# Performance work log

Measured on AMD Instinct MI355X. Metric: run time of the kernel, lower is better.

## Reference

```python
import jax, jax.numpy as jnp
import numpy as np
import math

DIM = 256; SEQ = 2048; BSZ = 32; NI = 128; NS = 4; ITERS = 3

def _ln(x, g, b):
    m = x.mean(-1, keepdims=True)
    v = ((x - m) ** 2).mean(-1, keepdims=True)
    return (x - m) / jnp.sqrt(v + 1e-5) * g + b

def _norm(x):
    # torch F.normalize: x / ||x||.clamp_min(1e-12)
    return x / jnp.clip(jnp.linalg.norm(x, axis=-1, keepdims=True), 1e-12, None)

def setup_inputs() -> dict:
    key = jax.random.key(0)
    ks = jax.random.split(key, 16)
    def w(k, shape, s=0.02):
        return jax.random.normal(k, shape, jnp.float32) * s
    return {
        'tokens': jax.random.normal(ks[0], (BSZ, SEQ, DIM), jnp.float32),
        'cls_embed': jax.random.normal(ks[1], (BSZ, DIM), jnp.float32),
        'intent_queries': jax.random.normal(ks[2], (NI, DIM), jnp.float32),
        'noise': jax.random.normal(ks[3], (NI, BSZ, NS, DIM), jnp.float32),
        'Wk': w(ks[4], (DIM, DIM)), 'bk': jnp.zeros(DIM, jnp.float32),
        'Wv': w(ks[5], (DIM, DIM)), 'bv': jnp.zeros(DIM, jnp.float32),
        'Wqs': w(ks[6], (DIM, DIM)), 'bqs': jnp.zeros(DIM, jnp.float32),
        'Wqi': w(ks[7], (DIM, DIM)), 'bqi': jnp.zeros(DIM, jnp.float32),
        'ln1_g': jnp.ones(DIM, jnp.float32), 'ln1_b': jnp.zeros(DIM, jnp.float32),
        'ln2_g': jnp.ones(DIM, jnp.float32), 'ln2_b': jnp.zeros(DIM, jnp.float32),
        'Wf1': w(ks[8], (DIM, 2 * DIM)), 'bf1': jnp.zeros(2 * DIM, jnp.float32),
        'Wf2': w(ks[9], (2 * DIM, DIM)), 'bf2': jnp.zeros(DIM, jnp.float32),
        'slot_mu': w(ks[10], (1, NS, DIM)),  # randn*0.02
        'slot_sigma': jnp.ones((1, NS, DIM), jnp.float32) * 0.1,
        'alpha': jnp.float32(1.0),
        'temperature': jnp.float32(1.0),
    }

def reference(tokens, cls_embed, intent_queries, noise, Wk, bk, Wv, bv,
              Wqs, bqs, Wqi, bqi, ln1_g, ln1_b, ln2_g, ln2_b,
              Wf1, bf1, Wf2, bf2, slot_mu, slot_sigma, alpha, temperature):
    scale = 1.0 / math.sqrt(DIM)
    # k/v are identical across the per-intent loop in the original -> compute once
    k = tokens @ Wk + bk  # [B,S,D]
    v = tokens @ Wv + bv  # [B,S,D]
    cls_n = _norm(cls_embed)  # [B,D]

    def per_intent(q, eps):  # q: [D], eps: [B,NS,D]
        qn = _norm(q)
        q_intent = (q @ Wqi + bqi)[None, None, :]  # broadcast over [B,NS,:]
        slots = slot_mu[0] + eps * slot_sigma[0]   # [B,NS,D]
        for _ in range(ITERS):
            q_slot = slots @ Wqs + bqs + q_intent
            logit = jnp.einsum('bnd,bsd->bns', q_slot, k) * scale
            attn = jax.nn.softmax(logit, axis=-1)
            upd = jnp.einsum('bns,bsd->bnd', attn, v)
            slots = _ln(slots + upd, ln1_g, ln1_b)
            h = _ln(slots, ln2_g, ln2_b)
            slots = slots + jax.nn.gelu(h @ Wf1 + bf1, approximate=False) @ Wf2 + bf2
        sn = _norm(slots)                               # [B,NS,D]
        a = jax.nn.softmax(jnp.einsum('bnd,d->bn', sn, qn), axis=-1)
        summ = jnp.einsum('bn,bnd->bd', a, slots)       # slot_summary
        fused = cls_n + alpha * _norm(summ)
        return fused @ qn                               # [B]

    scores = jax.vmap(per_intent)(intent_queries, noise)  # [NI,B]
    logits = scores.T / jnp.maximum(temperature, 1e-4)    # [B,NI]
    return logits
```

## Files before the change

### kernel.cpp

```cpp
#include <hip/hip_runtime.h>
#include <math.h>

#define BSZ 32
#define NI  128

typedef __attribute__((ext_vector_type(8))) _Float16 f16x8;
typedef __attribute__((ext_vector_type(4))) _Float16 f16x4;
typedef __attribute__((ext_vector_type(4))) float    f32x4;

#define MFMA16(a, b, c) __builtin_amdgcn_mfma_f32_16x16x32_f16((a), (b), (c), 0, 0, 0)

#define GLL(g, l) __builtin_amdgcn_global_load_lds(                          \
    (const __attribute__((address_space(1))) void*)(g),                      \
    (__attribute__((address_space(3))) void*)(l), 16, 0, 0)

#define LGKM_BAR() do {                                                      \
    asm volatile("s_waitcnt lgkmcnt(0)" ::: "memory");                       \
    __builtin_amdgcn_sched_barrier(0);                                       \
    __builtin_amdgcn_s_barrier();                                            \
    __builtin_amdgcn_sched_barrier(0); } while (0)

__device__ inline float dot4f(float4 a, float4 b) {
    return a.x * b.x + a.y * b.y + a.z * b.z + a.w * b.w;
}

__device__ inline float4* slp(float* base, int r, int c) {
    return (float4*)(base + r * 256 + ((((c) >> 2) ^ (r & 7)) << 2));
}

__device__ inline void tpose64(const float* __restrict__ src, int Csrc,
                               _Float16* __restrict__ dstT, int KT,
                               int r0, int c0, _Float16 (*tbuf)[72], int tid)
{
#pragma unroll
    for (int it = 0; it < 4; it++) {
        int idx = tid + it * 256;
        int rr = idx >> 4, c4 = idx & 15;
        float4 w = *(const float4*)(src + (size_t)(r0 + rr) * Csrc + c0 + c4 * 4);
        tbuf[c4 * 4 + 0][rr] = (_Float16)w.x;
        tbuf[c4 * 4 + 1][rr] = (_Float16)w.y;
        tbuf[c4 * 4 + 2][rr] = (_Float16)w.z;
        tbuf[c4 * 4 + 3][rr] = (_Float16)w.w;
    }
    __syncthreads();
#pragma unroll
    for (int it = 0; it < 2; it++) {
        int idx = tid + it * 256;
        int orr = idx >> 3, oc8 = idx & 7;
        int n = c0 + orr;
        size_t tile = (size_t)(n >> 4) * KT + (r0 >> 5) + (oc8 >> 2);
        *(f16x8*)(dstT + tile * 512 + (n & 15) * 32 + (oc8 & 3) * 8) = *(const f16x8*)&tbuf[orr][oc8 * 8];
    }
}

__global__ __launch_bounds__(256) void prep(
    const float* __restrict__ Wk, const float* __restrict__ Wv,
    const float* __restrict__ Wqs, const float* __restrict__ Wf1,
    const float* __restrict__ Wf2,
    const float* __restrict__ intent_q, const float* __restrict__ Wqi,
    const float* __restrict__ bqi, const float* __restrict__ bqs,
    const float* __restrict__ cls_embed,
    _Float16* __restrict__ wkT, _Float16* __restrict__ wvT,
    _Float16* __restrict__ wqsT, _Float16* __restrict__ wf1T,
    _Float16* __restrict__ wf2T,
    float* __restrict__ qint2, float* __restrict__ qn, float* __restrict__ clsn)
{
    __shared__ _Float16 tbuf[64][72];
    __shared__ float buf[256];
    __shared__ float red[4];
    const int t = threadIdx.x, blk = blockIdx.x;
    const int lane = t & 63, w = t >> 6;

    if (blk < 112) {
        if (blk < 16)       tpose64(Wk, 256, wkT, 8, (blk >> 2) * 64, (blk & 3) * 64, tbuf, t);
        else if (blk < 32)  { int tt = blk - 16; tpose64(Wv, 256, wvT, 8, (tt >> 2) * 64, (tt & 3) * 64, tbuf, t); }
        else if (blk < 48)  { int tt = blk - 32; tpose64(Wqs, 256, wqsT, 8, (tt >> 2) * 64, (tt & 3) * 64, tbuf, t); }
        else if (blk < 80)  { int tt = blk - 48; tpose64(Wf1, 512, wf1T, 8, (tt & 3) * 64, (tt >> 2) * 64, tbuf, t); }
        else                { int tt = blk - 80; tpose64(Wf2, 256, wf2T, 16, (tt >> 2) * 64, (tt & 3) * 64, tbuf, t); }
    } else if (blk < 240) {
        int i = blk - 112;
        float x = intent_q[(size_t)i * 256 + t];
        buf[t] = x;
        float ss = x * x;
#pragma unroll
        for (int m = 1; m < 64; m <<= 1) ss += __shfl_xor(ss, m, 64);
        if (lane == 0) red[w] = ss;
        __syncthreads();
        float tot = red[0] + red[1] + red[2] + red[3];
        qn[(size_t)i * 256 + t] = x / fmaxf(sqrtf(tot), 1e-12f);
        float acc = bqi[t] + bqs[t];
        for (int e = 0; e < 256; e += 4) {
            const float4 q4 = *(const float4*)&buf[e];
            acc += q4.x * Wqi[(size_t)(e + 0) * 256 + t];
            acc += q4.y * Wqi[(size_t)(e + 1) * 256 + t];
            acc += q4.z * Wqi[(size_t)(e + 2) * 256 + t];
            acc += q4.w * Wqi[(size_t)(e + 3) * 256 + t];
        }
        qint2[(size_t)i * 256 + t] = acc;
    } else {
        int b = blk - 240;
        float x = cls_embed[(size_t)b * 256 + t];
        float ss = x * x;
#pragma unroll
        for (int m = 1; m < 64; m <<= 1) ss += __shfl_xor(ss, m, 64);
        if (lane == 0) red[w] = ss;
        __syncthreads();
        float tot = red[0] + red[1] + red[2] + red[3];
        clsn[(size_t)b * 256 + t] = x / fmaxf(sqrtf(tot), 1e-12f);
    }
}

__global__ __launch_bounds__(512, 2) void kvf_k(
    const float* __restrict__ tokens,
    const _Float16* __restrict__ wkT, const _Float16* __restrict__ wvT,
    const float* __restrict__ bk, const float* __restrict__ bv,
    _Float16* __restrict__ kT, _Float16* __restrict__ vT)
{
    __shared__ __align__(16) _Float16 Sb[2][8192];

    const int t = threadIdx.x, lane = t & 63, w = t >> 6;
    const int l15 = lane & 15, quad = lane >> 4;
    const int lofs = l15 * 32 + quad * 8;
    const int lofsA = ((l15 * 4 + quad) ^ ((l15 >> 1) & 7)) * 8;
    const int bx = blockIdx.x;
    const int b = bx & 31, chunk = bx >> 5;

    f16x8 wk[2][8], wv[2][8];
#pragma unroll
    for (int j = 0; j < 2; j++)
#pragma unroll
        for (int ks = 0; ks < 8; ks++) {
            wk[j][ks] = *(const f16x8*)(wkT + ((size_t)(2 * w + j) * 8 + ks) * 512 + lofs);
            wv[j][ks] = *(const f16x8*)(wvT + ((size_t)(2 * w + j) * 8 + ks) * 512 + lofs);
        }
    f32x4 bi0 = *(const f32x4*)(bk + w * 32 + quad * 4);
    f32x4 bi1 = *(const f32x4*)(bk + w * 32 + 16 + quad * 4);
    const float bv0 = bv[(2 * w) * 16 + l15];
    const float bv1 = bv[(2 * w + 1) * 16 + l15];

    const int rr = t >> 5, d8 = t & 31;
    const float* tbase = tokens + ((size_t)b * 2048 + chunk * 256) * 256 + rr * 256 + d8 * 8;
    const int mskW = ((rr >> 1) & 7) ^ (((d8 >> 2) & 3) << 1);
    const int wofs0 = (d8 >> 2) * 512 + (((rr * 4 + (d8 & 3)) ^ mskW) * 8);
    const int wofs1 = wofs0 + 8 * 512;

    float4 pa0, pa1, pb0, pb1;

#define KVF_LOADS(P) do {                                                    \
        const float* sp_ = tbase + (size_t)(P) * 8192;                       \
        pa0 = *(const float4*)(sp_);                                         \
        pa1 = *(const float4*)(sp_ + 4);                                     \
        pb0 = *(const float4*)(sp_ + 4096);                                  \
        pb1 = *(const float4*)(sp_ + 4100);                                  \
    } while (0)

#define KVF_STAGE(BUF) do {                                                  \
        f16x8 h0, h1;                                                        \
        h0[0] = (_Float16)pa0.x; h0[1] = (_Float16)pa0.y;                    \
        h0[2] = (_Float16)pa0.z; h0[3] = (_Float16)pa0.w;                    \
        h0[4] = (_Float16)pa1.x; h0[5] = (_Float16)pa1.y;                    \
        h0[6] = (_Float16)pa1.z; h0[7] = (_Float16)pa1.w;                    \
        h1[0] = (_Float16)pb0.x; h1[1] = (_Float16)pb0.y;                    \
        h1[2] = (_Float16)pb0.z; h1[3] = (_Float16)pb0.w;                    \
        h1[4] = (_Float16)pb1.x; h1[5] = (_Float16)pb1.y;                    \
        h1[6] = (_Float16)pb1.z; h1[7] = (_Float16)pb1.w;                    \
        *(f16x8*)((BUF) + wofs0) = h0;                                       \
        *(f16x8*)((BUF) + wofs1) = h1;                                       \
    } while (0)

    KVF_LOADS(0);
    KVF_STAGE(&Sb[0][0]);
    LGKM_BAR();

    for (int p = 0; p < 8; p++) {
        if (p < 7) KVF_LOADS(p + 1);
        __builtin_amdgcn_sched_barrier(0);

        const _Float16* lb = &Sb[p & 1][0];
        const int stg0 = chunk * 16 + p * 2;
        const int sp = chunk * 8 + p;

        f16x8 a[2][8];
#pragma unroll
        for (int st = 0; st < 2; st++)
#pragma unroll
            for (int ks = 0; ks < 8; ks++)
                a[st][ks] = *(const f16x8*)(lb + (st * 8 + ks) * 512 + (lofsA ^ ((ks & 3) * 16)));

#pragma unroll
        for (int st = 0; st < 2; st++) {
            f32x4 c0 = {0.f, 0.f, 0.f, 0.f}, c1 = {0.f, 0.f, 0.f, 0.f};
#pragma unroll
            for (int ks = 0; ks < 8; ks++) {
                c0 = MFMA16(wk[0][ks], a[st][ks], c0);
                c1 = MFMA16(wk[1][ks], a[st][ks], c1);
            }
            f16x4 p0, p1;
#pragma unroll
            for (int reg = 0; reg < 4; reg++) {
                p0[reg] = (_Float16)(c0[reg] + bi0[reg]);
                p1[reg] = (_Float16)(c1[reg] + bi1[reg]);
            }
            _Float16* tp = kT + ((size_t)(b * 128 + stg0 + st) * 8 + w) * 512 + l15 * 32;
            *(f16x4*)(tp + (quad >> 1) * 8 + (quad & 1) * 4) = p0;
            *(f16x4*)(tp + (2 + (quad >> 1)) * 8 + (quad & 1) * 4) = p1;
        }

#pragma unroll
        for (int j = 0; j < 2; j++) {
            f32x4 c0 = {0.f, 0.f, 0.f, 0.f}, c1 = {0.f, 0.f, 0.f, 0.f};
#pragma unroll
            for (int ks = 0; ks < 8; ks++) {
                c0 = MFMA16(a[0][ks], wv[j][ks], c0);
                c1 = MFMA16(a[1][ks], wv[j][ks], c1);
            }
            const float bb = j ? bv1 : bv0;
            f16x4 p0, p1;
#pragma unroll
            for (int reg = 0; reg < 4; reg++) {
                p0[reg] = (_Float16)(c0[reg] + bb);
                p1[reg] = (_Float16)(c1[reg] + bb);
            }
            _Float16* tp = vT + ((size_t)(b * 16 + 2 * w + j) * 64 + sp) * 512 + l15 * 32;
            *(f16x4*)(tp + (quad >> 1) * 8 + (quad & 1) * 4) = p0;
            *(f16x4*)(tp + (2 + (quad >> 1)) * 8 + (quad & 1) * 4) = p1;
        }

        if (p < 7) {
            KVF_STAGE(&Sb[(p + 1) & 1][0]);
            LGKM_BAR();
        }
    }
#undef KVF_LOADS
#undef KVF_STAGE
}

__global__ __launch_bounds__(256) void slots_init(
    const float* __restrict__ noise, const float* __restrict__ slot_mu,
    const float* __restrict__ slot_sigma, float* __restrict__ slots,
    _Float16* __restrict__ slotsT)
{
    int idx = blockIdx.x * 256 + threadIdx.x;
    int row = idx >> 5, d8 = idx & 31;
    int b = row >> 9, i = (row >> 2) & 127, n = row & 3;
    int d = d8 * 8;
    const float* mp = slot_mu + n * 256 + d;
    const float* sp = slot_sigma + n * 256 + d;
    const float* np = noise + (((size_t)i * BSZ + b) * 4 + n) * 256 + d;
    float4 o0, o1;
    {
        float4 mu = *(const float4*)mp, sg = *(const float4*)sp, ns = *(const float4*)np;
        o0.x = mu.x + ns.x * sg.x; o0.y = mu.y + ns.y * sg.y;
        o0.z = mu.z + ns.z * sg.z; o0.w = mu.w + ns.w * sg.w;
    }
    {
        float4 mu = *(const float4*)(mp + 4), sg = *(const float4*)(sp + 4), ns = *(const float4*)(np + 4);
        o1.x = mu.x + ns.x * sg.x; o1.y = mu.y + ns.y * sg.y;
        o1.z = mu.z + ns.z * sg.z; o1.w = mu.w + ns.w * sg.w;
    }
    *(float4*)(slots + (size_t)row * 256 + d) = o0;
    *(float4*)(slots + (size_t)row * 256 + d + 4) = o1;
    f16x8 h;
    h[0] = (_Float16)o0.x; h[1] = (_Float16)o0.y; h[2] = (_Float16)o0.z; h[3] = (_Float16)o0.w;
    h[4] = (_Float16)o1.x; h[5] = (_Float16)o1.y; h[6] = (_Float16)o1.z; h[7] = (_Float16)o1.w;
    *(f16x8*)(slotsT + ((size_t)(row >> 4) * 8 + (d8 >> 2)) * 512 + (row & 15) * 32 + (d8 & 3) * 8) = h;
}

__global__ __launch_bounds__(256) void qslot_k(
    const _Float16* __restrict__ slotsT, const _Float16* __restrict__ wqsT,
    const float* __restrict__ qint2, _Float16* __restrict__ qsT)
{
    const int tid = threadIdx.x, lane = tid & 63, wv = tid >> 6;
    const int l15 = lane & 15, quad = lane >> 4;
    const int lofs = l15 * 32 + quad * 8;
    const int bx = blockIdx.x, rb = bx >> 2, dq = bx & 3;
    const int rt = rb * 4 + wv;
    const int gr0 = rt * 16;

    f16x8 bs[8];
#pragma unroll
    for (int ks = 0; ks < 8; ks++)
        bs[ks] = *(const f16x8*)(slotsT + ((size_t)rt * 8 + ks) * 512 + lofs);
    const int iq = ((gr0 + l15) & 511) >> 2;
#pragma unroll
    for (int dt = 0; dt < 4; dt++) {
        int dti = dq * 4 + dt;
        f32x4 c = {0.f, 0.f, 0.f, 0.f};
#pragma unroll
        for (int ks = 0; ks < 8; ks++)
            c = MFMA16(*(const f16x8*)(wqsT + ((size_t)dti * 8 + ks) * 512 + lofs), bs[ks], c);
        float4 qi = *(const float4*)(qint2 + (size_t)iq * 256 + dti * 16 + quad * 4);
        f16x4 o;
#pragma unroll
        for (int reg = 0; reg < 4; reg++) o[reg] = (_Float16)((c[reg] + qi[reg]) * 0.0625f);
        *(f16x4*)(qsT + ((size_t)rt * 8 + (dti >> 1)) * 512 + l15 * 32
                  + ((dti & 1) * 2 + (quad >> 1)) * 8 + (quad & 1) * 4) = o;
    }
}

__global__ __launch_bounds__(512, 2) void attn_k(
    const _Float16* __restrict__ qsT, const _Float16* __restrict__ kT,
    const _Float16* __restrict__ vT,
    _Float16* __restrict__ Opart, float* __restrict__ psum4)
{
    __shared__ __align__(16) _Float16 Kb[2][16384];
    __shared__ __align__(16) _Float16 Vb[16384];
    __shared__ __align__(16) _Float16 pb[8][2304];

    const int tid = threadIdx.x, lane = tid & 63, wv = tid >> 6;
    const int l15 = lane & 15, quad = lane >> 4;
    const int lofs = l15 * 32 + quad * 8;
    const int lofsA = ((l15 * 4 + quad) ^ ((l15 >> 1) & 7)) * 8;
    const int lnsw = (lane ^ ((lane >> 3) & 7)) * 8;
    const int bx = blockIdx.x;
    const int b = bx & 31, rb = (bx >> 5) & 1, sk = bx >> 6;
    const int gr0 = b * 512 + rb * 256 + wv * 32;
    const int rt_q = gr0 >> 4;

    _Float16* pw = pb[wv];

    const _Float16* kSrc = kT + ((size_t)(b * 128 + sk * 32) * 8) * 512;

    {
        const _Float16* src = kSrc + (size_t)(wv * 4) * 512 + lnsw;
        _Float16* dst = &Kb[0][(wv * 4) * 512 + lane * 8];
#pragma unroll
        for (int j = 0; j < 4; j++) GLL(src + j * 512, dst + j * 512);
    }

    f16x8 q[2][8];
#pragma unroll
    for (int m = 0; m < 2; m++)
#pragma unroll
        for (int ks = 0; ks < 8; ks++)
            q[m][ks] = *(const f16x8*)(qsT + ((size_t)(rt_q + m) * 8 + ks) * 512 + lofs);

    f32x4 O[2][16];
#pragma unroll
    for (int m = 0; m < 2; m++)
#pragma unroll
        for (int dt = 0; dt < 16; dt++) O[m][dt] = (f32x4){0.f, 0.f, 0.f, 0.f};
    float ps[2][4] = {{0.f, 0.f, 0.f, 0.f}, {0.f, 0.f, 0.f, 0.f}};

    asm volatile("s_waitcnt vmcnt(0)" ::: "memory");
    __builtin_amdgcn_s_barrier();
    __builtin_amdgcn_sched_barrier(0);

    for (int s = 0; s < 8; s++) {
        const int cur = s & 1;

        {
            const int seg0 = wv * 4;
#pragma unroll
            for (int j = 0; j < 4; j++) {
                const int seg = seg0 + j;
                const _Float16* src = vT
                    + ((size_t)(b * 16 + (seg >> 1)) * 64 + sk * 16 + s * 2 + (seg & 1)) * 512
                    + lnsw;
                GLL(src, &Vb[seg * 512 + lane * 8]);
            }
        }
        if (s < 7) {
            const _Float16* src = kSrc + (size_t)(s + 1) * 16384 + (wv * 4) * 512 + lnsw;
            _Float16* dst = &Kb[cur ^ 1][(wv * 4) * 512 + lane * 8];
#pragma unroll
            for (int j = 0; j < 4; j++) GLL(src + j * 512, dst + j * 512);
            asm volatile("s_waitcnt vmcnt(8)" ::: "memory");
        } else {
            asm volatile("s_waitcnt vmcnt(4)" ::: "memory");
        }
        __builtin_amdgcn_s_barrier();
        __builtin_amdgcn_sched_barrier(0);

#pragma unroll
        for (int kt = 0; kt < 4; kt++) {
            const _Float16* kp = &Kb[cur][(kt * 8) * 512];
            f32x4 c0 = {0.f, 0.f, 0.f, 0.f}, c1 = {0.f, 0.f, 0.f, 0.f};
#pragma unroll
            for (int ks = 0; ks < 8; ks++) {
                f16x8 kf = *(const f16x8*)(kp + ks * 512 + lofsA);
                c0 = MFMA16(q[0][ks], kf, c0);
                c1 = MFMA16(q[1][ks], kf, c1);
            }
            const int col = kt * 16 + l15;
#pragma unroll
            for (int reg = 0; reg < 4; reg++) {
                float p0 = __expf(fminf(c0[reg], 10.5f));
                float p1 = __expf(fminf(c1[reg], 10.5f));
                ps[0][reg] += p0;
                ps[1][reg] += p1;
                pw[(quad * 4 + reg) * 72 + col] = (_Float16)p0;
                pw[(16 + quad * 4 + reg) * 72 + col] = (_Float16)p1;
            }
        }

        __builtin_amdgcn_sched_barrier(0);
        if (s < 7) {
            asm volatile("s_waitcnt vmcnt(4)" ::: "memory");
        } else {
            asm volatile("s_waitcnt vmcnt(0)" ::: "memory");
        }
        __builtin_amdgcn_s_barrier();
        __builtin_amdgcn_sched_barrier(0);

        f16x8 pa[2][2];
#pragma unroll
        for (int m = 0; m < 2; m++)
#pragma unroll
            for (int kg = 0; kg < 2; kg++)
                pa[m][kg] = *(const f16x8*)(pw + (m * 16 + l15) * 72 + kg * 32 + quad * 8);
#pragma unroll
        for (int dt = 0; dt < 16; dt++) {
            const _Float16* vp = &Vb[dt * 1024];
            f16x8 v0 = *(const f16x8*)(vp + lofsA);
            f16x8 v1 = *(const f16x8*)(vp + 512 + lofsA);
            O[0][dt] = MFMA16(pa[0][0], v0, O[0][dt]);
            O[0][dt] = MFMA16(pa[0][1], v1, O[0][dt]);
            O[1][dt] = MFMA16(pa[1][0], v0, O[1][dt]);
            O[1][dt] = MFMA16(pa[1][1], v1, O[1][dt]);
        }

        __builtin_amdgcn_sched_barrier(0);
        __builtin_amdgcn_s_barrier();
        __builtin_amdgcn_sched_barrier(0);
    }

#pragma unroll
    for (int m = 0; m < 2; m++) {
#pragma unroll
        for (int msk = 1; msk <= 8; msk <<= 1)
#pragma unroll
            for (int reg = 0; reg < 4; reg++) ps[m][reg] += __shfl_xor(ps[m][reg], msk, 64);
        if (l15 == 0) {
#pragma unroll
            for (int reg = 0; reg < 4; reg++)
                psum4[(size_t)sk * 16384 + gr0 + m * 16 + quad * 4 + reg] = ps[m][reg];
        }
    }

#pragma unroll
    for (int m = 0; m < 2; m++) {
#pragma unroll
        for (int hd = 0; hd < 2; hd++) {
#pragma unroll
            for (int dt = 0; dt < 8; dt++) {
                const int dti = hd * 8 + dt;
#pragma unroll
                for (int reg = 0; reg < 4; reg++)
                    pw[(quad * 4 + reg) * 136 + dt * 16 + l15] = (_Float16)O[m][dti][reg];
            }
#pragma unroll
            for (int p2 = 0; p2 < 4; p2++) {
                const int u = lane + p2 * 64;
                const int row = u >> 4, col8 = u & 15;
                *(f16x8*)(Opart + ((size_t)sk * 16384 + gr0 + m * 16 + row) * 256 + hd * 128 + col8 * 8) =
                    *(const f16x8*)(pw + row * 136 + col8 * 8);
            }
        }
    }
}

__global__ __launch_bounds__(256, 2) void mlp_k(
    const _Float16* __restrict__ Opart, const float* __restrict__ psum4,
    float* __restrict__ slots,
    const float* __restrict__ ln1_g, const float* __restrict__ ln1_b,
    const float* __restrict__ ln2_g, const float* __restrict__ ln2_b,
    const _Float16* __restrict__ wf1T, const float* __restrict__ bf1,
    const _Float16* __restrict__ wf2T, const float* __restrict__ bf2,
    const _Float16* __restrict__ wqsT, const float* __restrict__ qint2,
    _Float16* __restrict__ qsT,
    const float* __restrict__ qn, const float* __restrict__ clsn,
    const float* __restrict__ alphap, const float* __restrict__ tempp,
    float* __restrict__ out, int it)
{
    __shared__ float sl[32 * 256];
    __shared__ float2 st2[32];
    __shared__ __align__(16) _Float16 actL[16384];

    const int tid = threadIdx.x, lane = tid & 63, w4 = tid >> 6;
    const int l15 = lane & 15, quad = lane >> 4;
    const int lofs = l15 * 32 + quad * 8;
    const int lofsA = ((l15 * 4 + quad) ^ ((l15 >> 1) & 7)) * 8;
    const int pairW = w4 >> 1, half = w4 & 1;
    const int bx = blockIdx.x;
    const int b = bx & 31, rg = bx >> 5;
    const int R0 = b * 512 + rg * 32;

#pragma unroll
    for (int r2 = 0; r2 < 2; r2++) {
        const int lr = w4 * 8 + r2 * 4 + quad;
        const int gr = R0 + lr;
        float l = 0.f;
#pragma unroll
        for (int j = 0; j < 4; j++) l += psum4[(size_t)j * 16384 + gr];
        const float invl = 1.f / l;
        float4 y[4];
        float sm = 0.f, sq = 0.f;
#pragma unroll
        for (int k = 0; k < 4; k++) {
            const int c = k * 64 + l15 * 4;
            float4 o4 = {0.f, 0.f, 0.f, 0.f};
#pragma unroll
            for (int j = 0; j < 4; j++) {
                f16x4 p = *(const f16x4*)(Opart + ((size_t)j * 16384 + gr) * 256 + c);
                o4.x += (float)p[0]; o4.y += (float)p[1];
                o4.z += (float)p[2]; o4.w += (float)p[3];
            }
            float4 s4 = *(const float4*)(slots + (size_t)gr * 256 + c);
            y[k].x = s4.x + o4.x * invl; y[k].y = s4.y + o4.y * invl;
            y[k].z = s4.z + o4.z * invl; y[k].w = s4.w + o4.w * invl;
            sm += y[k].x + y[k].y + y[k].z + y[k].w;
            sq += dot4f(y[k], y[k]);
        }
#pragma unroll
        for (int m = 1; m <= 8; m <<= 1) { sm += __shfl_xor(sm, m, 64); sq += __shfl_xor(sq, m, 64); }
        const float mean = sm * (1.f / 256.f);
        const float rstd = rsqrtf(sq * (1.f / 256.f) - mean * mean + 1e-5f);
        float sm2 = 0.f, sq2 = 0.f;
#pragma unroll
        for (int k = 0; k < 4; k++) {
            const int c = k * 64 + l15 * 4;
            float4 g1 = *(const float4*)(ln1_g + c);
            float4 b1 = *(const float4*)(ln1_b + c);
            float4 x1;
            x1.x = (y[k].x - mean) * rstd * g1.x + b1.x;
            x1.y = (y[k].y - mean) * rstd * g1.y + b1.y;
            x1.z = (y[k].z - mean) * rstd * g1.z + b1.z;
            x1.w = (y[k].w - mean) * rstd * g1.w + b1.w;
            *slp(sl, lr, c) = x1;
            sm2 += x1.x + x1.y + x1.z + x1.w;
            sq2 += dot4f(x1, x1);
        }
#pragma unroll
        for (int m = 1; m <= 8; m <<= 1) { sm2 += __shfl_xor(sm2, m, 64); sq2 += __shfl_xor(sq2, m, 64); }
        const float mean2 = sm2 * (1.f / 256.f);
        const float rstd2 = rsqrtf(sq2 * (1.f / 256.f) - mean2 * mean2 + 1e-5f);
        if (l15 == 0) st2[lr] = make_float2(mean2, rstd2);
    }
    __syncthreads();

    const int lrf = pairW * 16 + l15;
    {
        const float2 s2 = st2[lrf];
        f16x8 bh[8];
#pragma unroll
        for (int ks = 0; ks < 8; ks++) {
            const int c0 = ks * 32 + quad * 8;
            float4 xa = *slp(sl, lrf, c0);
            float4 xb = *slp(sl, lrf, c0 + 4);
            float4 ga = *(const float4*)(ln2_g + c0);
            float4 gb = *(const float4*)(ln2_g + c0 + 4);
            float4 ba = *(const float4*)(ln2_b + c0);
            float4 bb2 = *(const float4*)(ln2_b + c0 + 4);
            bh[ks][0] = (_Float16)((xa.x - s2.x) * s2.y * ga.x + ba.x);
            bh[ks][1] = (_Float16)((xa.y - s2.x) * s2.y * ga.y + ba.y);
            bh[ks][2] = (_Float16)((xa.z - s2.x) * s2.y * ga.z + ba.z);
            bh[ks][3] = (_Float16)((xa.w - s2.x) * s2.y * ga.w + ba.w);
            bh[ks][4] = (_Float16)((xb.x - s2.x) * s2.y * gb.x + bb2.x);
            bh[ks][5] = (_Float16)((xb.y - s2.x) * s2.y * gb.y + bb2.y);
            bh[ks][6] = (_Float16)((xb.z - s2.x) * s2.y * gb.z + bb2.z);
            bh[ks][7] = (_Float16)((xb.w - s2.x) * s2.y * gb.w + bb2.w);
        }
#pragma unroll 2
        for (int t16 = 0; t16 < 16; t16++) {
            const int hti = half * 16 + t16;
            f32x4 c = {0.f, 0.f, 0.f, 0.f};
#pragma unroll
            for (int ks = 0; ks < 8; ks++)
                c = MFMA16(*(const f16x8*)(wf1T + ((size_t)hti * 8 + ks) * 512 + lofs), bh[ks], c);
            float4 bb = *(const float4*)(bf1 + hti * 16 + quad * 4);
            f16x4 o;
#pragma unroll
            for (int reg = 0; reg < 4; reg++) {
                float xg = c[reg] + bb[reg];
                o[reg] = (_Float16)(0.5f * xg * (1.f + erff(xg * 0.70710678118654752f)));
            }
            const int gA = l15 * 4 + (hti & 1) * 2 + (quad >> 1);
            *(f16x4*)(actL + ((size_t)(pairW * 16 + (hti >> 1))) * 512
                      + ((gA ^ ((l15 >> 1) & 7)) * 8) + (quad & 1) * 4) = o;
        }
    }
    __syncthreads();

    {
        f32x4 c[8];
#pragma unroll
        for (int d = 0; d < 8; d++) {
            const int dti = half * 8 + d;
            float4 x4 = *slp(sl, lrf, dti * 16 + quad * 4);
            float4 bb = *(const float4*)(bf2 + dti * 16 + quad * 4);
            c[d] = (f32x4){x4.x + bb.x, x4.y + bb.y, x4.z + bb.z, x4.w + bb.w};
        }
        const _Float16* ap = actL + ((size_t)pairW * 16) * 512;
        for (int ks = 0; ks < 16; ks++) {
            f16x8 afrag = *(const f16x8*)(ap + (size_t)ks * 512 + lofsA);
#pragma unroll
            for (int d = 0; d < 8; d++)
                c[d] = MFMA16(*(const f16x8*)(wf2T + ((size_t)(half * 8 + d) * 16 + ks) * 512 + lofs),
                              afrag, c[d]);
        }
#pragma unroll
        for (int d = 0; d < 8; d++) {
            const int dti = half * 8 + d;
            float4 v = {c[d][0], c[d][1], c[d][2], c[d][3]};
            *slp(sl, lrf, dti * 16 + quad * 4) = v;
        }
    }
    __syncthreads();

    if (it < 2) {
        f16x8 bs[8];
#pragma unroll
        for (int ks = 0; ks < 8; ks++) {
            const int c0 = ks * 32 + quad * 8;
            float4 xa = *slp(sl, lrf, c0);
            float4 xb = *slp(sl, lrf, c0 + 4);
            bs[ks][0] = (_Float16)xa.x; bs[ks][1] = (_Float16)xa.y;
            bs[ks][2] = (_Float16)xa.z; bs[ks][3] = (_Float16)xa.w;
            bs[ks][4] = (_Float16)xb.x; bs[ks][5] = (_Float16)xb.y;
            bs[ks][6] = (_Float16)xb.z; bs[ks][7] = (_Float16)xb.w;
        }
        const int iq = (rg * 32 + pairW * 16 + l15) >> 2;
        const int rtg = b * 32 + rg * 2 + pairW;
#pragma unroll
        for (int d = 0; d < 8; d++) {
            const int dti = half * 8 + d;
            f32x4 c = {0.f, 0.f, 0.f, 0.f};
#pragma unroll
            for (int ks = 0; ks < 8; ks++)
                c = MFMA16(*(const f16x8*)(wqsT + ((size_t)dti * 8 + ks) * 512 + lofs), bs[ks], c);
            float4 qi = *(const float4*)(qint2 + (size_t)iq * 256 + dti * 16 + quad * 4);
            f16x4 o;
#pragma unroll
            for (int reg = 0; reg < 4; reg++) o[reg] = (_Float16)((c[reg] + qi[reg]) * 0.0625f);
            *(f16x4*)(qsT + ((size_t)rtg * 8 + (dti >> 1)) * 512 + l15 * 32
                      + ((dti & 1) * 2 + (quad >> 1)) * 8 + (quad & 1) * 4) = o;
        }
        {
            const int lr2 = tid >> 3, k8 = tid & 7;
#pragma unroll
            for (int q4 = 0; q4 < 8; q4++) {
                float4 v = *slp(sl, lr2, k8 * 32 + q4 * 4);
                *(float4*)(slots + (size_t)(R0 + lr2) * 256 + k8 * 32 + q4 * 4) = v;
            }
        }
    } else {
#pragma unroll
        for (int ii = 0; ii < 2; ii++) {
            const int i_loc = w4 * 2 + ii;
            const int i = rg * 8 + i_loc;
            float4 qv = *(const float4*)(qn + (size_t)i * 256 + lane * 4);
            float4 xs[4];
            float st4[4];
#pragma unroll
            for (int n = 0; n < 4; n++) {
                xs[n] = *slp(sl, i_loc * 4 + n, lane * 4);
                float ss = dot4f(xs[n], xs[n]);
                float sq = dot4f(xs[n], qv);
#pragma unroll
                for (int m = 1; m < 64; m <<= 1) { ss += __shfl_xor(ss, m, 64); sq += __shfl_xor(sq, m, 64); }
                st4[n] = sq / fmaxf(sqrtf(ss), 1e-12f);
            }
            float mx = fmaxf(fmaxf(st4[0], st4[1]), fmaxf(st4[2], st4[3]));
            float e0 = __expf(st4[0] - mx), e1 = __expf(st4[1] - mx);
            float e2 = __expf(st4[2] - mx), e3 = __expf(st4[3] - mx);
            float inv = 1.f / (e0 + e1 + e2 + e3);
            float4 smv;
            smv.x = (e0 * xs[0].x + e1 * xs[1].x + e2 * xs[2].x + e3 * xs[3].x) * inv;
            smv.y = (e0 * xs[0].y + e1 * xs[1].y + e2 * xs[2].y + e3 * xs[3].y) * inv;
            smv.z = (e0 * xs[0].z + e1 * xs[1].z + e2 * xs[2].z + e3 * xs[3].z) * inv;
            smv.w = (e0 * xs[0].w + e1 * xs[1].w + e2 * xs[2].w + e3 * xs[3].w) * inv;
            float ssm = dot4f(smv, smv);
            float sqn = dot4f(smv, qv);
            float4 cv = *(const float4*)(clsn + (size_t)b * 256 + lane * 4);
            float cq = dot4f(cv, qv);
#pragma unroll
            for (int m = 1; m < 64; m <<= 1) {
                ssm += __shfl_xor(ssm, m, 64);
                sqn += __shfl_xor(sqn, m, 64);
                cq  += __shfl_xor(cq,  m, 64);
            }
            if (lane == 0) {
                float score = cq + alphap[0] * sqn / fmaxf(sqrtf(ssm), 1e-12f);
                out[(size_t)b * NI + i] = score / fmaxf(tempp[0], 1e-4f);
            }
        }
    }
}

extern "C" void kernel_launch(void* const* d_in, const int* in_sizes, int n_in,
                              void* d_out, int out_size, void* d_ws, size_t ws_size,
                              hipStream_t stream)
{
    const float* tokens     = (const float*)d_in[0];
    const float* cls_embed  = (const float*)d_in[1];
    const float* intent_q   = (const float*)d_in[2];
    const float* noise      = (const float*)d_in[3];
    const float* Wk  = (const float*)d_in[4];
    const float* bk  = (const float*)d_in[5];
    const float* Wv  = (const float*)d_in[6];
    const float* bv  = (const float*)d_in[7];
    const float* Wqs = (const float*)d_in[8];
    const float* bqs = (const float*)d_in[9];
    const float* Wqi = (const float*)d_in[10];
    const float* bqi = (const float*)d_in[11];
    const float* ln1g = (const float*)d_in[12];
    const float* ln1b = (const float*)d_in[13];
    const float* ln2g = (const float*)d_in[14];
    const float* ln2b = (const float*)d_in[15];
    const float* Wf1 = (const float*)d_in[16];
    const float* bf1 = (const float*)d_in[17];
    const float* Wf2 = (const float*)d_in[18];
    const float* bf2 = (const float*)d_in[19];
    const float* slot_mu    = (const float*)d_in[20];
    const float* slot_sigma = (const float*)d_in[21];
    const float* alphap = (const float*)d_in[22];
    const float* tempp  = (const float*)d_in[23];
    float* out = (float*)d_out;

    char* base = (char*)d_ws;
    _Float16* qsT   = (_Float16*)(base);
    _Float16* slotsT= (_Float16*)(base + 8388608u);
    _Float16* kT    = (_Float16*)(base + 33554432u);
    _Float16* vT    = (_Float16*)(base + 67108864u);
    _Float16* Opart = (_Float16*)(base + 100663296u);
    float* slots    = (float*)(base + 134217728u);
    _Float16* wkT   = (_Float16*)(base + 150994944u);
    _Float16* wvT   = (_Float16*)(base + 151126016u);
    _Float16* wqsT  = (_Float16*)(base + 151257088u);
    _Float16* wf1T  = (_Float16*)(base + 151388160u);
    _Float16* wf2T  = (_Float16*)(base + 151650304u);
    float* qint2    = (float*)(base + 151912448u);
    float* qnb      = (float*)(base + 152043520u);
    float* clsn     = (float*)(base + 152174592u);
    float* psum4    = (float*)(base + 152207360u);

    prep<<<272, 256, 0, stream>>>(Wk, Wv, Wqs, Wf1, Wf2, intent_q, Wqi, bqi, bqs,
                                  cls_embed, wkT, wvT, wqsT, wf1T, wf2T,
                                  qint2, qnb, clsn);
    kvf_k<<<256, 512, 0, stream>>>(tokens, wkT, wvT, bk, bv, kT, vT);
    slots_init<<<2048, 256, 0, stream>>>(noise, slot_mu, slot_sigma, slots, slotsT);
    qslot_k<<<1024, 256, 0, stream>>>(slotsT, wqsT, qint2, qsT);

    for (int it = 0; it < 3; it++) {
        attn_k<<<256, 512, 0, stream>>>(qsT, kT, vT, Opart, psum4);
        mlp_k<<<512, 256, 0, stream>>>(Opart, psum4, slots,
                                       ln1g, ln1b, ln2g, ln2b,
                                       wf1T, bf1, wf2T, bf2,
                                       wqsT, qint2, qsT,
                                       qnb, clsn, alphap, tempp, out, it);
    }
}
```

Measured before the change: 490.0 us.

## Fuse slot init, q-projection, attention and MLP iterations into one persistent kernel

Replaces the separate slots_init, qslot_k and the per-iteration attn_k/mlp_k launches with a single mega_k kernel. Each block keeps its 64 slot rows in LDS across all three iterations and streams the full K/V sequence for its batch itself. This removes the global round-trips for slots, qsT, Opart and psum4 and cuts the launch count. In exchange the sequence is no longer split across blocks (previously 4 splits), so each block runs a long serial 64-step loop with fewer MFMAs per barrier. Only 256 blocks run, which risks lower parallelism and latency-bound attention.

Result: slower. 843.7 us (+72.2%).

```diff
diff --git a/kernel.cpp b/kernel.cpp
--- a/kernel.cpp
+++ b/kernel.cpp
@@ -235,56 +235,27 @@
 #undef KVF_STAGE
 }
 
-__global__ __launch_bounds__(256) void slots_init(
-    const float* __restrict__ noise, const float* __restrict__ slot_mu,
-    const float* __restrict__ slot_sigma, float* __restrict__ slots,
-    _Float16* __restrict__ slotsT)
+__device__ inline void qs_phase(float* sl, _Float16* qsA,
+                                const _Float16* __restrict__ wqsT,
+                                const float* __restrict__ qint2,
+                                int rt, int h, int l15, int quad, int lofs, int R0)
 {
-    int idx = blockIdx.x * 256 + threadIdx.x;
-    int row = idx >> 5, d8 = idx & 31;
-    int b = row >> 9, i = (row >> 2) & 127, n = row & 3;
-    int d = d8 * 8;
-    const float* mp = slot_mu + n * 256 + d;
-    const float* sp = slot_sigma + n * 256 + d;
-    const float* np = noise + (((size_t)i * BSZ + b) * 4 + n) * 256 + d;
-    float4 o0, o1;
-    {
-        float4 mu = *(const float4*)mp, sg = *(const float4*)sp, ns = *(const float4*)np;
-        o0.x = mu.x + ns.x * sg.x; o0.y = mu.y + ns.y * sg.y;
-        o0.z = mu.z + ns.z * sg.z; o0.w = mu.w + ns.w * sg.w;
-    }
-    {
-        float4 mu = *(const float4*)(mp + 4), sg = *(const float4*)(sp + 4), ns = *(const float4*)(np + 4);
-        o1.x = mu.x + ns.x * sg.x; o1.y = mu.y + ns.y * sg.y;
-        o1.z = mu.z + ns.z * sg.z; o1.w = mu.w + ns.w * sg.w;
-    }
-    *(float4*)(slots + (size_t)row * 256 + d) = o0;
-    *(float4*)(slots + (size_t)row * 256 + d + 4) = o1;
-    f16x8 h;
-    h[0] = (_Float16)o0.x; h[1] = (_Float16)o0.y; h[2] = (_Float16)o0.z; h[3] = (_Float16)o0.w;
-    h[4] = (_Float16)o1.x; h[5] = (_Float16)o1.y; h[6] = (_Float16)o1.z; h[7] = (_Float16)o1.w;
-    *(f16x8*)(slotsT + ((size_t)(row >> 4) * 8 + (d8 >> 2)) * 512 + (row & 15) * 32 + (d8 & 3) * 8) = h;
-}
-
-__global__ __launch_bounds__(256) void qslot_k(
-    const _Float16* __restrict__ slotsT, const _Float16* __restrict__ wqsT,
-    const float* __restrict__ qint2, _Float16* __restrict__ qsT)
-{
-    const int tid = threadIdx.x, lane = tid & 63, wv = tid >> 6;
-    const int l15 = lane & 15, quad = lane >> 4;
-    const int lofs = l15 * 32 + quad * 8;
-    const int bx = blockIdx.x, rb = bx >> 2, dq = bx & 3;
-    const int rt = rb * 4 + wv;
-    const int gr0 = rt * 16;
-
+    const int lrf = rt * 16 + l15;
     f16x8 bs[8];
 #pragma unroll
-    for (int ks = 0; ks < 8; ks++)
-        bs[ks] = *(const f16x8*)(slotsT + ((size_t)rt * 8 + ks) * 512 + lofs);
-    const int iq = ((gr0 + l15) & 511) >> 2;
-#pragma unroll
-    for (int dt = 0; dt < 4; dt++) {
-        int dti = dq * 4 + dt;
+    for (int ks = 0; ks < 8; ks++) {
+        const int c0 = ks * 32 + quad * 8;
+        float4 xa = *slp(sl, lrf, c0);
+        float4 xb = *slp(sl, lrf, c0 + 4);
+        bs[ks][0] = (_Float16)xa.x; bs[ks][1] = (_Float16)xa.y;
+        bs[ks][2] = (_Float16)xa.z; bs[ks][3] = (_Float16)xa.w;
+        bs[ks][4] = (_Float16)xb.x; bs[ks][5] = (_Float16)xb.y;
+        bs[ks][6] = (_Float16)xb.z; bs[ks][7] = (_Float16)xb.w;
+    }
+    const int iq = ((R0 + lrf) >> 2) & 127;
+#pragma unroll
+    for (int d = 0; d < 8; d++) {
+        const int dti = h * 8 + d;
         f32x4 c = {0.f, 0.f, 0.f, 0.f};
 #pragma unroll
         for (int ks = 0; ks < 8; ks++)
@@ -293,397 +264,330 @@
         f16x4 o;
 #pragma unroll
         for (int reg = 0; reg < 4; reg++) o[reg] = (_Float16)((c[reg] + qi[reg]) * 0.0625f);
-        *(f16x4*)(qsT + ((size_t)rt * 8 + (dti >> 1)) * 512 + l15 * 32
+        *(f16x4*)(qsA + rt * 4096 + (dti >> 1) * 512 + l15 * 32
                   + ((dti & 1) * 2 + (quad >> 1)) * 8 + (quad & 1) * 4) = o;
     }
 }
 
-__global__ __launch_bounds__(512, 2) void attn_k(
-    const _Float16* __restrict__ qsT, const _Float16* __restrict__ kT,
-    const _Float16* __restrict__ vT,
-    _Float16* __restrict__ Opart, float* __restrict__ psum4)
+__global__ __launch_bounds__(512, 2) void mega_k(
+    const _Float16* __restrict__ kT, const _Float16* __restrict__ vT,
+    const float* __restrict__ noise, const float* __restrict__ slot_mu,
+    const float* __restrict__ slot_sigma,
+    const _Float16* __restrict__ wqsT, const float* __restrict__ qint2,
+    const float* __restrict__ ln1_g, const float* __restrict__ ln1_b,
+    const float* __restrict__ ln2_g, const float* __restrict__ ln2_b,
+    const _Float16* __restrict__ wf1T, const float* __restrict__ bf1,
+    const _Float16* __restrict__ wf2T, const float* __restrict__ bf2,
+    const float* __restrict__ qn, const float* __restrict__ clsn,
+    const float* __restrict__ alphap, const float* __restrict__ tempp,
+    float* __restrict__ out)
 {
-    __shared__ __align__(16) _Float16 Kb[2][16384];
-    __shared__ __align__(16) _Float16 Vb[16384];
-    __shared__ __align__(16) _Float16 pb[8][2304];
-
-    const int tid = threadIdx.x, lane = tid & 63, wv = tid >> 6;
+    __shared__ float sl[64 * 256];
+    __shared__ __align__(16) char arena[65536];
+    __shared__ float2 st2[64];
+    __shared__ float psb[2][64];
+
+    _Float16* KbA  = (_Float16*)arena;
+    _Float16* VbA  = (_Float16*)(arena + 32768);
+    _Float16* pbA  = (_Float16*)(arena + 49152);
+    float*    Obuf = (float*)arena;
+    _Float16* qsA  = (_Float16*)arena;
+    _Float16* actA = (_Float16*)arena;
+
+    const int tid = threadIdx.x, lane = tid & 63, wvid = tid >> 6;
     const int l15 = lane & 15, quad = lane >> 4;
     const int lofs = l15 * 32 + quad * 8;
     const int lofsA = ((l15 * 4 + quad) ^ ((l15 >> 1) & 7)) * 8;
     const int lnsw = (lane ^ ((lane >> 3) & 7)) * 8;
     const int bx = blockIdx.x;
-    const int b = bx & 31, rb = (bx >> 5) & 1, sk = bx >> 6;
-    const int gr0 = b * 512 + rb * 256 + wv * 32;
-    const int rt_q = gr0 >> 4;
-
-    _Float16* pw = pb[wv];
-
-    const _Float16* kSrc = kT + ((size_t)(b * 128 + sk * 32) * 8) * 512;
+    const int b = bx & 31, rg = bx >> 5;
+    const int R0 = b * 512 + rg * 64;
+    const int rt = wvid >> 1, h = wvid & 1;
 
     {
-        const _Float16* src = kSrc + (size_t)(wv * 4) * 512 + lnsw;
-        _Float16* dst = &Kb[0][(wv * 4) * 512 + lane * 8];
-#pragma unroll
-        for (int j = 0; j < 4; j++) GLL(src + j * 512, dst + j * 512);
-    }
-
-    f16x8 q[2][8];
-#pragma unroll
-    for (int m = 0; m < 2; m++)
+        const int lr = tid >> 3, f = tid & 7;
+        const int gr = R0 + lr;
+        const int ii = (gr >> 2) & 127, n = gr & 3;
+        const float* np = noise + (((size_t)ii * BSZ + b) * 4 + n) * 256;
+#pragma unroll
+        for (int j = 0; j < 8; j++) {
+            const int c = f * 32 + j * 4;
+            float4 mu = *(const float4*)(slot_mu + n * 256 + c);
+            float4 sg = *(const float4*)(slot_sigma + n * 256 + c);
+            float4 ns = *(const float4*)(np + c);
+            float4 o;
+            o.x = mu.x + ns.x * sg.x; o.y = mu.y + ns.y * sg.y;
+            o.z = mu.z + ns.z * sg.z; o.w = mu.w + ns.w * sg.w;
+            *slp(sl, lr, c) = o;
+        }
+    }
+    __syncthreads();
+
+    qs_phase(sl, qsA, wqsT, qint2, rt, h, l15, quad, lofs, R0);
+    __syncthreads();
+
+    for (int it = 0; it < 3; it++) {
+        f16x8 q[8];
 #pragma unroll
         for (int ks = 0; ks < 8; ks++)
-            q[m][ks] = *(const f16x8*)(qsT + ((size_t)(rt_q + m) * 8 + ks) * 512 + lofs);
-
-    f32x4 O[2][16];
-#pragma unroll
-    for (int m = 0; m < 2; m++)
-#pragma unroll
-        for (int dt = 0; dt < 16; dt++) O[m][dt] = (f32x4){0.f, 0.f, 0.f, 0.f};
-    float ps[2][4] = {{0.f, 0.f, 0.f, 0.f}, {0.f, 0.f, 0.f, 0.f}};
-
-    asm volatile("s_waitcnt vmcnt(0)" ::: "memory");
-    __builtin_amdgcn_s_barrier();
-    __builtin_amdgcn_sched_barrier(0);
-
-    for (int s = 0; s < 8; s++) {
-        const int cur = s & 1;
-
-        {
-            const int seg0 = wv * 4;
-#pragma unroll
-            for (int j = 0; j < 4; j++) {
-                const int seg = seg0 + j;
-                const _Float16* src = vT
-                    + ((size_t)(b * 16 + (seg >> 1)) * 64 + sk * 16 + s * 2 + (seg & 1)) * 512
-                    + lnsw;
-                GLL(src, &Vb[seg * 512 + lane * 8]);
-            }
-        }
-        if (s < 7) {
-            const _Float16* src = kSrc + (size_t)(s + 1) * 16384 + (wv * 4) * 512 + lnsw;
-            _Float16* dst = &Kb[cur ^ 1][(wv * 4) * 512 + lane * 8];
-#pragma unroll
-            for (int j = 0; j < 4; j++) GLL(src + j * 512, dst + j * 512);
-            asm volatile("s_waitcnt vmcnt(8)" ::: "memory");
-        } else {
-            asm volatile("s_waitcnt vmcnt(4)" ::: "memory");
-        }
+            q[ks] = *(const f16x8*)(qsA + rt * 4096 + ks * 512 + lofs);
+        __syncthreads();
+
+        f32x4 O[8];
+#pragma unroll
+        for (int d = 0; d < 8; d++) O[d] = (f32x4){0.f, 0.f, 0.f, 0.f};
+        float ps[4] = {0.f, 0.f, 0.f, 0.f};
+
+#pragma unroll
+        for (int j = 0; j < 2; j++) {
+            const int e = wvid * 2 + j;
+            GLL(kT + ((size_t)(b * 128 + (e >> 3)) * 8 + (e & 7)) * 512 + lnsw,
+                KbA + e * 512 + lane * 8);
+        }
+        asm volatile("s_waitcnt vmcnt(0)" ::: "memory");
         __builtin_amdgcn_s_barrier();
         __builtin_amdgcn_sched_barrier(0);
 
-#pragma unroll
-        for (int kt = 0; kt < 4; kt++) {
-            const _Float16* kp = &Kb[cur][(kt * 8) * 512];
-            f32x4 c0 = {0.f, 0.f, 0.f, 0.f}, c1 = {0.f, 0.f, 0.f, 0.f};
+        for (int ss = 0; ss < 64; ss++) {
+            const int cur = ss & 1;
+#pragma unroll
+            for (int j = 0; j < 2; j++) {
+                const int e = wvid * 2 + j;
+                GLL(vT + ((size_t)(b * 16 + e) * 64 + ss) * 512 + lnsw,
+                    VbA + e * 512 + lane * 8);
+            }
+            if (ss < 63) {
+#pragma unroll
+                for (int j = 0; j < 2; j++) {
+                    const int e = wvid * 2 + j;
+                    GLL(kT + ((size_t)(b * 128 + (ss + 1) * 2 + (e >> 3)) * 8 + (e & 7)) * 512 + lnsw,
+                        KbA + (cur ^ 1) * 8192 + e * 512 + lane * 8);
+                }
+                asm volatile("s_waitcnt vmcnt(4)" ::: "memory");
+            } else {
+                asm volatile("s_waitcnt vmcnt(2)" ::: "memory");
+            }
+            __builtin_amdgcn_s_barrier();
+            __builtin_amdgcn_sched_barrier(0);
+
+            {
+                const _Float16* kp = KbA + cur * 8192 + (h * 8) * 512;
+                f32x4 c0 = {0.f, 0.f, 0.f, 0.f};
+#pragma unroll
+                for (int ks = 0; ks < 8; ks++)
+                    c0 = MFMA16(q[ks], *(const f16x8*)(kp + ks * 512 + lofsA), c0);
+                _Float16* pw = pbA + rt * 640;
+#pragma unroll
+                for (int reg = 0; reg < 4; reg++) {
+                    float p0 = __expf(fminf(c0[reg], 10.5f));
+                    ps[reg] += p0;
+                    pw[(quad * 4 + reg) * 40 + h * 16 + l15] = (_Float16)p0;
+                }
+            }
+            __builtin_amdgcn_sched_barrier(0);
+            asm volatile("s_waitcnt lgkmcnt(0)" ::: "memory");
+            if (ss < 63) {
+                asm volatile("s_waitcnt vmcnt(2)" ::: "memory");
+            } else {
+                asm volatile("s_waitcnt vmcnt(0)" ::: "memory");
+            }
+            __builtin_amdgcn_s_barrier();
+            __builtin_amdgcn_sched_barrier(0);
+
+            {
+                const _Float16* pw = pbA + rt * 640;
+                f16x8 pa = *(const f16x8*)(pw + l15 * 40 + quad * 8);
+#pragma unroll
+                for (int d = 0; d < 8; d++) {
+                    const _Float16* vp = VbA + (h * 8 + d) * 512;
+                    O[d] = MFMA16(pa, *(const f16x8*)(vp + lofsA), O[d]);
+                }
+            }
+            __builtin_amdgcn_sched_barrier(0);
+            __builtin_amdgcn_s_barrier();
+            __builtin_amdgcn_sched_barrier(0);
+        }
+
+#pragma unroll
+        for (int msk = 1; msk <= 8; msk <<= 1)
+#pragma unroll
+            for (int reg = 0; reg < 4; reg++) ps[reg] += __shfl_xor(ps[reg], msk, 64);
+        if (l15 == 0) {
+#pragma unroll
+            for (int reg = 0; reg < 4; reg++)
+                psb[h][rt * 16 + quad * 4 + reg] = ps[reg];
+        }
+        __syncthreads();
+
+#pragma unroll
+        for (int d = 0; d < 8; d++) {
+            const int dt = h * 8 + d;
+#pragma unroll
+            for (int reg = 0; reg < 4; reg++) {
+                const int row = rt * 16 + quad * 4 + reg;
+                const int c = dt * 16 + l15;
+                Obuf[row * 256 + ((((c >> 2) ^ (row & 7)) << 2) | (c & 3))] = O[d][reg];
+            }
+        }
+        __syncthreads();
+
+#pragma unroll
+        for (int r2 = 0; r2 < 2; r2++) {
+            const int lr = rt * 16 + h * 8 + r2 * 4 + quad;
+            const float l = psb[0][lr] + psb[1][lr];
+            const float invl = 1.f / l;
+            float4 y[4];
+            float sm = 0.f, sq = 0.f;
+#pragma unroll
+            for (int k = 0; k < 4; k++) {
+                const int c = k * 64 + l15 * 4;
+                float4 o4 = *slp(Obuf, lr, c);
+                float4 s4 = *slp(sl, lr, c);
+                y[k].x = s4.x + o4.x * invl; y[k].y = s4.y + o4.y * invl;
+                y[k].z = s4.z + o4.z * invl; y[k].w = s4.w + o4.w * invl;
+                sm += y[k].x + y[k].y + y[k].z + y[k].w;
+                sq += dot4f(y[k], y[k]);
+            }
+#pragma unroll
+            for (int m = 1; m <= 8; m <<= 1) { sm += __shfl_xor(sm, m, 64); sq += __shfl_xor(sq, m, 64); }
+            const float mean = sm * (1.f / 256.f);
+            const float rstd = rsqrtf(sq * (1.f / 256.f) - mean * mean + 1e-5f);
+            float sm2 = 0.f, sq2 = 0.f;
+#pragma unroll
+            for (int k = 0; k < 4; k++) {
+                const int c = k * 64 + l15 * 4;
+                float4 g1 = *(const float4*)(ln1_g + c);
+                float4 b1 = *(const float4*)(ln1_b + c);
+                float4 x1;
+                x1.x = (y[k].x - mean) * rstd * g1.x + b1.x;
+                x1.y = (y[k].y - mean) * rstd * g1.y + b1.y;
+                x1.z = (y[k].z - mean) * rstd * g1.z + b1.z;
+                x1.w = (y[k].w - mean) * rstd * g1.w + b1.w;
+                *slp(sl, lr, c) = x1;
+                sm2 += x1.x + x1.y + x1.z + x1.w;
+                sq2 += dot4f(x1, x1);
+            }
+#pragma unroll
+            for (int m = 1; m <= 8; m <<= 1) { sm2 += __shfl_xor(sm2, m, 64); sq2 += __shfl_xor(sq2, m, 64); }
+            const float mean2 = sm2 * (1.f / 256.f);
+            const float rstd2 = rsqrtf(sq2 * (1.f / 256.f) - mean2 * mean2 + 1e-5f);
+            if (l15 == 0) st2[lr] = make_float2(mean2, rstd2);
+        }
+        __syncthreads();
+
+        const int lrf = rt * 16 + l15;
+        {
+            const float2 s2 = st2[lrf];
+            f16x8 bh[8];
 #pragma unroll
             for (int ks = 0; ks < 8; ks++) {
-                f16x8 kf = *(const f16x8*)(kp + ks * 512 + lofsA);
-                c0 = MFMA16(q[0][ks], kf, c0);
-                c1 = MFMA16(q[1][ks], kf, c1);
-            }
-            const int col = kt * 16 + l15;
-#pragma unroll
-            for (int reg = 0; reg < 4; reg++) {
-                float p0 = __expf(fminf(c0[reg], 10.5f));
-                float p1 = __expf(fminf(c1[reg], 10.5f));
-                ps[0][reg] += p0;
-                ps[1][reg] += p1;
-                pw[(quad * 4 + reg) * 72 + col] = (_Float16)p0;
-                pw[(16 + quad * 4 + reg) * 72 + col] = (_Float16)p1;
-            }
-        }
-
-        __builtin_amdgcn_sched_barrier(0);
-        if (s < 7) {
-            asm volatile("s_waitcnt vmcnt(4)" ::: "memory");
-        } else {
-            asm volatile("s_waitcnt vmcnt(0)" ::: "memory");
-        }
-        __builtin_amdgcn_s_barrier();
-        __builtin_amdgcn_sched_barrier(0);
-
-        f16x8 pa[2][2];
-#pragma unroll
-        for (int m = 0; m < 2; m++)
-#pragma unroll
-            for (int kg = 0; kg < 2; kg++)
-                pa[m][kg] = *(const f16x8*)(pw + (m * 16 + l15) * 72 + kg * 32 + quad * 8);
-#pragma unroll
-        for (int dt = 0; dt < 16; dt++) {
-            const _Float16* vp = &Vb[dt * 1024];
-            f16x8 v0 = *(const f16x8*)(vp + lofsA);
-            f16x8 v1 = *(const f16x8*)(vp + 512 + lofsA);
-            O[0][dt] = MFMA16(pa[0][0], v0, O[0][dt]);
-            O[0][dt] = MFMA16(pa[0][1], v1, O[0][dt]);
-            O[1][dt] = MFMA16(pa[1][0], v0, O[1][dt]);
-            O[1][dt] = MFMA16(pa[1][1], v1, O[1][dt]);
-        }
-
-        __builtin_amdgcn_sched_barrier(0);
-        __builtin_amdgcn_s_barrier();
-        __builtin_amdgcn_sched_barrier(0);
-    }
-
-#pragma unroll
-    for (int m = 0; m < 2; m++) {
-#pragma unroll
-        for (int msk = 1; msk <= 8; msk <<= 1)
-#pragma unroll
-            for (int reg = 0; reg < 4; reg++) ps[m][reg] += __shfl_xor(ps[m][reg], msk, 64);
-        if (l15 == 0) {
-#pragma unroll
-            for (int reg = 0; reg < 4; reg++)
-                psum4[(size_t)sk * 16384 + gr0 + m * 16 + quad * 4 + reg] = ps[m][reg];
-        }
-    }
-
-#pragma unroll
-    for (int m = 0; m < 2; m++) {
-#pragma unroll
-        for (int hd = 0; hd < 2; hd++) {
-#pragma unroll
-            for (int dt = 0; dt < 8; dt++) {
-                const int dti = hd * 8 + dt;
-#pragma unroll
-                for (int reg = 0; reg < 4; reg++)
-                    pw[(quad * 4 + reg) * 136 + dt * 16 + l15] = (_Float16)O[m][dti][reg];
-            }
-#pragma unroll
-            for (int p2 = 0; p2 < 4; p2++) {
-                const int u = lane + p2 * 64;
-                const int row = u >> 4, col8 = u & 15;
-                *(f16x8*)(Opart + ((size_t)sk * 16384 + gr0 + m * 16 + row) * 256 + hd * 128 + col8 * 8) =
-                    *(const f16x8*)(pw + row * 136 + col8 * 8);
-            }
-        }
-    }
-}
-
-__global__ __launch_bounds__(256, 2) void mlp_k(
-    const _Float16* __restrict__ Opart, const float* __restrict__ psum4,
-    float* __restrict__ slots,
-    const float* __restrict__ ln1_g, const float* __restrict__ ln1_b,
-    const float* __restrict__ ln2_g, const float* __restrict__ ln2_b,
-    const _Float16* __restrict__ wf1T, const float* __restrict__ bf1,
-    const _Float16* __restrict__ wf2T, const float* __restrict__ bf2,
-    const _Float16* __restrict__ wqsT, const float* __restrict__ qint2,
-    _Float16* __restrict__ qsT,
-    const float* __restrict__ qn, const float* __restrict__ clsn,
-    const float* __restrict__ alphap, const float* __restrict__ tempp,
-    float* __restrict__ out, int it)
-{
-    __shared__ float sl[32 * 256];
-    __shared__ float2 st2[32];
-    __shared__ __align__(16) _Float16 actL[16384];
-
-    const int tid = threadIdx.x, lane = tid & 63, w4 = tid >> 6;
-    const int l15 = lane & 15, quad = lane >> 4;
-    const int lofs = l15 * 32 + quad * 8;
-    const int lofsA = ((l15 * 4 + quad) ^ ((l15 >> 1) & 7)) * 8;
-    const int pairW = w4 >> 1, half = w4 & 1;
-    const int bx = blockIdx.x;
-    const int b = bx & 31, rg = bx >> 5;
-    const int R0 = b * 512 + rg * 32;
-
-#pragma unroll
-    for (int r2 = 0; r2 < 2; r2++) {
-        const int lr = w4 * 8 + r2 * 4 + quad;
-        const int gr = R0 + lr;
-        float l = 0.f;
-#pragma unroll
-        for (int j = 0; j < 4; j++) l += psum4[(size_t)j * 16384 + gr];
-        const float invl = 1.f / l;
-        float4 y[4];
-        float sm = 0.f, sq = 0.f;
-#pragma unroll
-        for (int k = 0; k < 4; k++) {
-            const int c = k * 64 + l15 * 4;
-            float4 o4 = {0.f, 0.f, 0.f, 0.f};
-#pragma unroll
-            for (int j = 0; j < 4; j++) {
-                f16x4 p = *(const f16x4*)(Opart + ((size_t)j * 16384 + gr) * 256 + c);
-                o4.x += (float)p[0]; o4.y += (float)p[1];
-                o4.z += (float)p[2]; o4.w += (float)p[3];
-            }
-            float4 s4 = *(const float4*)(slots + (size_t)gr * 256 + c);
-            y[k].x = s4.x + o4.x * invl; y[k].y = s4.y + o4.y * invl;
-            y[k].z = s4.z + o4.z * invl; y[k].w = s4.w + o4.w * invl;
-            sm += y[k].x + y[k].y + y[k].z + y[k].w;
-            sq += dot4f(y[k], y[k]);
-        }
-#pragma unroll
-        for (int m = 1; m <= 8; m <<= 1) { sm += __shfl_xor(sm, m, 64); sq += __shfl_xor(sq, m, 64); }
-        const float mean = sm * (1.f / 256.f);
-        const float rstd = rsqrtf(sq * (1.f / 256.f) - mean * mean + 1e-5f);
-        float sm2 = 0.f, sq2 = 0.f;
-#pragma unroll
-        for (int k = 0; k < 4; k++) {
-            const int c = k * 64 + l15 * 4;
-            float4 g1 = *(const float4*)(ln1_g + c);
-            float4 b1 = *(const float4*)(ln1_b + c);
-            float4 x1;
-            x1.x = (y[k].x - mean) * rstd * g1.x + b1.x;
-            x1.y = (y[k].y - mean) * rstd * g1.y + b1.y;
-            x1.z = (y[k].z - mean) * rstd * g1.z + b1.z;
-            x1.w = (y[k].w - mean) * rstd * g1.w + b1.w;
-            *slp(sl, lr, c) = x1;
-            sm2 += x1.x + x1.y + x1.z + x1.w;
-            sq2 += dot4f(x1, x1);
-        }
-#pragma unroll
-        for (int m = 1; m <= 8; m <<= 1) { sm2 += __shfl_xor(sm2, m, 64); sq2 += __shfl_xor(sq2, m, 64); }
-        const float mean2 = sm2 * (1.f / 256.f);
-        const float rstd2 = rsqrtf(sq2 * (1.f / 256.f) - mean2 * mean2 + 1e-5f);
-        if (l15 == 0) st2[lr] = make_float2(mean2, rstd2);
-    }
-    __syncthreads();
-
-    const int lrf = pairW * 16 + l15;
-    {
-        const float2 s2 = st2[lrf];
-        f16x8 bh[8];
-#pragma unroll
-        for (int ks = 0; ks < 8; ks++) {
-            const int c0 = ks * 32 + quad * 8;
-            float4 xa = *slp(sl, lrf, c0);
-            float4 xb = *slp(sl, lrf, c0 + 4);
-            float4 ga = *(const float4*)(ln2_g + c0);
-            float4 gb = *(const float4*)(ln2_g + c0 + 4);
-            float4 ba = *(const float4*)(ln2_b + c0);
-            float4 bb2 = *(const float4*)(ln2_b + c0 + 4);
-            bh[ks][0] = (_Float16)((xa.x - s2.x) * s2.y * ga.x + ba.x);
-            bh[ks][1] = (_Float16)((xa.y - s2.x) * s2.y * ga.y + ba.y);
-            bh[ks][2] = (_Float16)((xa.z - s2.x) * s2.y * ga.z + ba.z);
-            bh[ks][3] = (_Float16)((xa.w - s2.x) * s2.y * ga.w + ba.w);
-            bh[ks][4] = (_Float16)((xb.x - s2.x) * s2.y * gb.x + bb2.x);
-            bh[ks][5] = (_Float16)((xb.y - s2.x) * s2.y * gb.y + bb2.y);
-            bh[ks][6] = (_Float16)((xb.z - s2.x) * s2.y * gb.z + bb2.z);
-            bh[ks][7] = (_Float16)((xb.w - s2.x) * s2.y * gb.w + bb2.w);
-        }
+                const int c0 = ks * 32 + quad * 8;
+                float4 xa = *slp(sl, lrf, c0);
+                float4 xb = *slp(sl, lrf, c0 + 4);
+                float4 ga = *(const float4*)(ln2_g + c0);
+                float4 gb = *(const float4*)(ln2_g + c0 + 4);
+                float4 ba = *(const float4*)(ln2_b + c0);
+                float4 bb2 = *(const float4*)(ln2_b + c0 + 4);
+                bh[ks][0] = (_Float16)((xa.x - s2.x) * s2.y * ga.x + ba.x);
+                bh[ks][1] = (_Float16)((xa.y - s2.x) * s2.y * ga.y + ba.y);
+                bh[ks][2] = (_Float16)((xa.z - s2.x) * s2.y * ga.z + ba.z);
+                bh[ks][3] = (_Float16)((xa.w - s2.x) * s2.y * ga.w + ba.w);
+                bh[ks][4] = (_Float16)((xb.x - s2.x) * s2.y * gb.x + bb2.x);
+                bh[ks][5] = (_Float16)((xb.y - s2.x) * s2.y * gb.y + bb2.y);
+                bh[ks][6] = (_Float16)((xb.z - s2.x) * s2.y * gb.z + bb2.z);
+                bh[ks][7] = (_Float16)((xb.w - s2.x) * s2.y * gb.w + bb2.w);
+            }
 #pragma unroll 2
-        for (int t16 = 0; t16 < 16; t16++) {
-            const int hti = half * 16 + t16;
-            f32x4 c = {0.f, 0.f, 0.f, 0.f};
-#pragma unroll
-            for (int ks = 0; ks < 8; ks++)
-                c = MFMA16(*(const f16x8*)(wf1T + ((size_t)hti * 8 + ks) * 512 + lofs), bh[ks], c);
-            float4 bb = *(const float4*)(bf1 + hti * 16 + quad * 4);
-            f16x4 o;
-#pragma unroll
-            for (int reg = 0; reg < 4; reg++) {
-                float xg = c[reg] + bb[reg];
-                o[reg] = (_Float16)(0.5f * xg * (1.f + erff(xg * 0.70710678118654752f)));
-            }
-            const int gA = l15 * 4 + (hti & 1) * 2 + (quad >> 1);
-            *(f16x4*)(actL + ((size_t)(pairW * 16 + (hti >> 1))) * 512
-                      + ((gA ^ ((l15 >> 1) & 7)) * 8) + (quad & 1) * 4) = o;
-        }
-    }
-    __syncthreads();
-
-    {
-        f32x4 c[8];
-#pragma unroll
-        for (int d = 0; d < 8; d++) {
-            const int dti = half * 8 + d;
-            float4 x4 = *slp(sl, lrf, dti * 16 + quad * 4);
-            float4 bb = *(const float4*)(bf2 + dti * 16 + quad * 4);
-            c[d] = (f32x4){x4.x + bb.x, x4.y + bb.y, x4.z + bb.z, x4.w + bb.w};
-        }
-        const _Float16* ap = actL + ((size_t)pairW * 16) * 512;
-        for (int ks = 0; ks < 16; ks++) {
-            f16x8 afrag = *(const f16x8*)(ap + (size_t)ks * 512 + lofsA);
-#pragma unroll
-            for (int d = 0; d < 8; d++)
-                c[d] = MFMA16(*(const f16x8*)(wf2T + ((size_t)(half * 8 + d) * 16 + ks) * 512 + lofs),
-                              afrag, c[d]);
-        }
-#pragma unroll
-        for (int d = 0; d < 8; d++) {
-            const int dti = half * 8 + d;
-            float4 v = {c[d][0], c[d][1], c[d][2], c[d][3]};
-            *slp(sl, lrf, dti * 16 + quad * 4) = v;
-        }
-    }
-    __syncthreads();
-
-    if (it < 2) {
-        f16x8 bs[8];
-#pragma unroll
-        for (int ks = 0; ks < 8; ks++) {
-            const int c0 = ks * 32 + quad * 8;
-            float4 xa = *slp(sl, lrf, c0);
-            float4 xb = *slp(sl, lrf, c0 + 4);
-            bs[ks][0] = (_Float16)xa.x; bs[ks][1] = (_Float16)xa.y;
-            bs[ks][2] = (_Float16)xa.z; bs[ks][3] = (_Float16)xa.w;
-            bs[ks][4] = (_Float16)xb.x; bs[ks][5] = (_Float16)xb.y;
-            bs[ks][6] = (_Float16)xb.z; bs[ks][7] = (_Float16)xb.w;
-        }
-        const int iq = (rg * 32 + pairW * 16 + l15) >> 2;
-        const int rtg = b * 32 + rg * 2 + pairW;
-#pragma unroll
-        for (int d = 0; d < 8; d++) {
-            const int dti = half * 8 + d;
-            f32x4 c = {0.f, 0.f, 0.f, 0.f};
-#pragma unroll
-            for (int ks = 0; ks < 8; ks++)
-                c = MFMA16(*(const f16x8*)(wqsT + ((size_t)dti * 8 + ks) * 512 + lofs), bs[ks], c);
-            float4 qi = *(const float4*)(qint2 + (size_t)iq * 256 + dti * 16 + quad * 4);
-            f16x4 o;
-#pragma unroll
-            for (int reg = 0; reg < 4; reg++) o[reg] = (_Float16)((c[reg] + qi[reg]) * 0.0625f);
-            *(f16x4*)(qsT + ((size_t)rtg * 8 + (dti >> 1)) * 512 + l15 * 32
-                      + ((dti & 1) * 2 + (quad >> 1)) * 8 + (quad & 1) * 4) = o;
-        }
+            for (int t16 = 0; t16 < 16; t16++) {
+                const int hti = h * 16 + t16;
+                f32x4 c = {0.f, 0.f, 0.f, 0.f};
+#pragma unroll
+                for (int ks = 0; ks < 8; ks++)
+                    c = MFMA16(*(const f16x8*)(wf1T + ((size_t)hti * 8 + ks) * 512 + lofs), bh[ks], c);
+                float4 bb = *(const float4*)(bf1 + hti * 16 + quad * 4);
+                f16x4 o;
+#pragma unroll
+                for (int reg = 0; reg < 4; reg++) {
+                    float xg = c[reg] + bb[reg];
+                    o[reg] = (_Float16)(0.5f * xg * (1.f + erff(xg * 0.70710678118654752f)));
+                }
+                const int gA = l15 * 4 + (hti & 1) * 2 + (quad >> 1);
+                *(f16x4*)(actA + rt * 8192 + ((size_t)(hti >> 1)) * 512
+                          + ((gA ^ ((l15 >> 1) & 7)) * 8) + (quad & 1) * 4) = o;
+            }
+        }
+        __syncthreads();
+
         {
-            const int lr2 = tid >> 3, k8 = tid & 7;
-#pragma unroll
-            for (int q4 = 0; q4 < 8; q4++) {
-                float4 v = *slp(sl, lr2, k8 * 32 + q4 * 4);
-                *(float4*)(slots + (size_t)(R0 + lr2) * 256 + k8 * 32 + q4 * 4) = v;
-            }
-        }
-    } else {
-#pragma unroll
-        for (int ii = 0; ii < 2; ii++) {
-            const int i_loc = w4 * 2 + ii;
-            const int i = rg * 8 + i_loc;
-            float4 qv = *(const float4*)(qn + (size_t)i * 256 + lane * 4);
-            float4 xs[4];
-            float st4[4];
-#pragma unroll
-            for (int n = 0; n < 4; n++) {
-                xs[n] = *slp(sl, i_loc * 4 + n, lane * 4);
-                float ss = dot4f(xs[n], xs[n]);
-                float sq = dot4f(xs[n], qv);
-#pragma unroll
-                for (int m = 1; m < 64; m <<= 1) { ss += __shfl_xor(ss, m, 64); sq += __shfl_xor(sq, m, 64); }
-                st4[n] = sq / fmaxf(sqrtf(ss), 1e-12f);
-            }
-            float mx = fmaxf(fmaxf(st4[0], st4[1]), fmaxf(st4[2], st4[3]));
-            float e0 = __expf(st4[0] - mx), e1 = __expf(st4[1] - mx);
-            float e2 = __expf(st4[2] - mx), e3 = __expf(st4[3] - mx);
-            float inv = 1.f / (e0 + e1 + e2 + e3);
-            float4 smv;
-            smv.x = (e0 * xs[0].x + e1 * xs[1].x + e2 * xs[2].x + e3 * xs[3].x) * inv;
-            smv.y = (e0 * xs[0].y + e1 * xs[1].y + e2 * xs[2].y + e3 * xs[3].y) * inv;
-            smv.z = (e0 * xs[0].z + e1 * xs[1].z + e2 * xs[2].z + e3 * xs[3].z) * inv;
-            smv.w = (e0 * xs[0].w + e1 * xs[1].w + e2 * xs[2].w + e3 * xs[3].w) * inv;
-            float ssm = dot4f(smv, smv);
-            float sqn = dot4f(smv, qv);
-            float4 cv = *(const float4*)(clsn + (size_t)b * 256 + lane * 4);
-            float cq = dot4f(cv, qv);
-#pragma unroll
-            for (int m = 1; m < 64; m <<= 1) {
-                ssm += __shfl_xor(ssm, m, 64);
-                sqn += __shfl_xor(sqn, m, 64);
-                cq  += __shfl_xor(cq,  m, 64);
-            }
-            if (lane == 0) {
-                float score = cq + alphap[0] * sqn / fmaxf(sqrtf(ssm), 1e-12f);
-                out[(size_t)b * NI + i] = score / fmaxf(tempp[0], 1e-4f);
-            }
+            f32x4 c[8];
+#pragma unroll
+            for (int d = 0; d < 8; d++) {
+                const int dti = h * 8 + d;
+                float4 x4 = *slp(sl, lrf, dti * 16 + quad * 4);
+                float4 bb = *(const float4*)(bf2 + dti * 16 + quad * 4);
+                c[d] = (f32x4){x4.x + bb.x, x4.y + bb.y, x4.z + bb.z, x4.w + bb.w};
+            }
+            for (int ks = 0; ks < 16; ks++) {
+                f16x8 afrag = *(const f16x8*)(actA + rt * 8192 + (size_t)ks * 512 + lofsA);
+#pragma unroll
+                for (int d = 0; d < 8; d++)
+                    c[d] = MFMA16(*(const f16x8*)(wf2T + ((size_t)(h * 8 + d) * 16 + ks) * 512 + lofs),
+                                  afrag, c[d]);
+            }
+            __syncthreads();
+#pragma unroll
+            for (int d = 0; d < 8; d++) {
+                const int dti = h * 8 + d;
+                float4 v = {c[d][0], c[d][1], c[d][2], c[d][3]};
+                *slp(sl, lrf, dti * 16 + quad * 4) = v;
+            }
+        }
+        __syncthreads();
+
+        if (it < 2) {
+            qs_phase(sl, qsA, wqsT, qint2, rt, h, l15, quad, lofs, R0);
+            __syncthreads();
+        }
+    }
+
+#pragma unroll
+    for (int ii = 0; ii < 2; ii++) {
+        const int i_loc = wvid * 2 + ii;
+        const int i = rg * 16 + i_loc;
+        float4 qv = *(const float4*)(qn + (size_t)i * 256 + lane * 4);
+        float4 xs[4];
+        float st4[4];
+#pragma unroll
+        for (int n = 0; n < 4; n++) {
+            xs[n] = *slp(sl, i_loc * 4 + n, lane * 4);
+            float ss = dot4f(xs[n], xs[n]);
+            float sq = dot4f(xs[n], qv);
+#pragma unroll
+            for (int m = 1; m < 64; m <<= 1) { ss += __shfl_xor(ss, m, 64); sq += __shfl_xor(sq, m, 64); }
+            st4[n] = sq / fmaxf(sqrtf(ss), 1e-12f);
+        }
+        float mx = fmaxf(fmaxf(st4[0], st4[1]), fmaxf(st4[2], st4[3]));
+        float e0 = __expf(st4[0] - mx), e1 = __expf(st4[1] - mx);
+        float e2 = __expf(st4[2] - mx), e3 = __expf(st4[3] - mx);
+        float inv = 1.f / (e0 + e1 + e2 + e3);
+        float4 smv;
+        smv.x = (e0 * xs[0].x + e1 * xs[1].x + e2 * xs[2].x + e3 * xs[3].x) * inv;
+        smv.y = (e0 * xs[0].y + e1 * xs[1].y + e2 * xs[2].y + e3 * xs[3].y) * inv;
+        smv.z = (e0 * xs[0].z + e1 * xs[1].z + e2 * xs[2].z + e3 * xs[3].z) * inv;
+        smv.w = (e0 * xs[0].w + e1 * xs[1].w + e2 * xs[2].w + e3 * xs[3].w) * inv;
+        float ssm = dot4f(smv, smv);
+        float sqn = dot4f(smv, qv);
+        float4 cv = *(const float4*)(clsn + (size_t)b * 256 + lane * 4);
+        float cq = dot4f(cv, qv);
+#pragma unroll
+        for (int m = 1; m < 64; m <<= 1) {
+            ssm += __shfl_xor(ssm, m, 64);
+            sqn += __shfl_xor(sqn, m, 64);
+            cq  += __shfl_xor(cq,  m, 64);
+        }
+        if (lane == 0) {
+            float score = cq + alphap[0] * sqn / fmaxf(sqrtf(ssm), 1e-12f);
+            out[(size_t)b * NI + i] = score / fmaxf(tempp[0], 1e-4f);
         }
     }
 }
@@ -719,12 +623,8 @@
     float* out = (float*)d_out;
 
     char* base = (char*)d_ws;
-    _Float16* qsT   = (_Float16*)(base);
-    _Float16* slotsT= (_Float16*)(base + 8388608u);
     _Float16* kT    = (_Float16*)(base + 33554432u);
     _Float16* vT    = (_Float16*)(base + 67108864u);
-    _Float16* Opart = (_Float16*)(base + 100663296u);
-    float* slots    = (float*)(base + 134217728u);
     _Float16* wkT   = (_Float16*)(base + 150994944u);
     _Float16* wvT   = (_Float16*)(base + 151126016u);
     _Float16* wqsT  = (_Float16*)(base + 151257088u);
@@ -733,21 +633,14 @@
     float* qint2    = (float*)(base + 151912448u);
     float* qnb      = (float*)(base + 152043520u);
     float* clsn     = (float*)(base + 152174592u);
-    float* psum4    = (float*)(base + 152207360u);
 
     prep<<<272, 256, 0, stream>>>(Wk, Wv, Wqs, Wf1, Wf2, intent_q, Wqi, bqi, bqs,
                                   cls_embed, wkT, wvT, wqsT, wf1T, wf2T,
                                   qint2, qnb, clsn);
     kvf_k<<<256, 512, 0, stream>>>(tokens, wkT, wvT, bk, bv, kT, vT);
-    slots_init<<<2048, 256, 0, stream>>>(noise, slot_mu, slot_sigma, slots, slotsT);
-    qslot_k<<<1024, 256, 0, stream>>>(slotsT, wqsT, qint2, qsT);
-
-    for (int it = 0; it < 3; it++) {
-        attn_k<<<256, 512, 0, stream>>>(qsT, kT, vT, Opart, psum4);
-        mlp_k<<<512, 256, 0, stream>>>(Opart, psum4, slots,
-                                       ln1g, ln1b, ln2g, ln2b,
-                                       wf1T, bf1, wf2T, bf2,
-                                       wqsT, qint2, qsT,
-                                       qnb, clsn, alphap, tempp, out, it);
-    }
-}
+    mega_k<<<256, 512, 0, stream>>>(kT, vT, noise, slot_mu, slot_sigma,
+                                    wqsT, qint2,
+                                    ln1g, ln1b, ln2g, ln2b,
+                                    wf1T, bf1, wf2T, bf2,
+                                    qnb, clsn, alphap, tempp, out);
+}
```
